# Kernel tuning notes

Hardware: AMD Instinct MI355X
Metric: run time of the kernel (lower is better)

The kernel has to match this reference:

```python
import jax, jax.numpy as jnp
import numpy as np

B, N, Q = 4, 4096, 4096
K = 32                    # max_neighbors (k = min(max_neighbors, N))
NUM_ATOM_TYPES = 100
EMBED_DIM = 32
RBF_DIM = 16
CUTOFF = 5.0
RBF_GAMMA = 1.0 / max(CUTOFF / max(RBF_DIM, 1), 1e-6) ** 2  # 10.24
EPS = 1e-12


def setup_inputs() -> dict:
    key = jax.random.key(0)
    k1, k2, k3, k4, k5 = jax.random.split(key, 5)
    coords = jax.random.normal(k1, (B, N, 3), dtype=jnp.float32) * 10.0
    atom_types = jax.random.randint(k2, (B, N), 0, NUM_ATOM_TYPES)
    radii = jax.random.uniform(k3, (B, N), dtype=jnp.float32) + 0.5
    query_points = jax.random.normal(k4, (B, Q, 3), dtype=jnp.float32) * 10.0
    atom_mask = jnp.ones((B, N), dtype=bool)
    query_mask = jnp.ones((B, Q), dtype=bool)
    embed_table = jax.random.normal(k5, (NUM_ATOM_TYPES, EMBED_DIM), dtype=jnp.float32)
    rbf_centers = jnp.linspace(0.0, CUTOFF, RBF_DIM, dtype=jnp.float32)
    return {"coords": coords, "atom_types": atom_types, "radii": radii,
            "query_points": query_points, "atom_mask": atom_mask,
            "query_mask": query_mask, "embed_table": embed_table,
            "rbf_centers": rbf_centers}


def reference(coords, atom_types, radii, query_points, atom_mask, query_mask,
              embed_table, rbf_centers):
    b = coords.shape[0]
    # stable pairwise distances [B, Q, N]
    diff = query_points[:, :, None, :] - coords[:, None, :, :]
    dists = jnp.sqrt(jnp.sum(diff * diff, axis=-1) + EPS)
    masked_dists = jnp.where(atom_mask[:, None, :], dists, jnp.inf)
    # smallest-k via top_k on negated distances -> [B, Q, K]
    neg_vals, sorted_indices = jax.lax.top_k(-masked_dists, K)
    sorted_dists = -neg_vals

    bidx = jnp.arange(b)[:, None, None]                       # [B,1,1]
    neighbor_atom_mask = atom_mask[bidx, sorted_indices]      # [B,Q,K]
    neighbor_mask = neighbor_atom_mask & (sorted_dists <= CUTOFF) & query_mask[:, :, None]

    neighbor_coords = coords[bidx, sorted_indices]            # [B,Q,K,3]
    neighbor_radii = radii[bidx, sorted_indices][..., None]   # [B,Q,K,1]
    neighbor_types = atom_types[bidx, sorted_indices]         # [B,Q,K]
    neighbor_emb = embed_table[neighbor_types]                # [B,Q,K,E]

    rel_pos = query_points[:, :, None, :] - neighbor_coords   # [B,Q,K,3]
    rel_dist = sorted_dists[..., None]                        # [B,Q,K,1]
    rbf = jnp.exp(-RBF_GAMMA * (rel_dist - rbf_centers[None, None, None, :]) ** 2)

    features = jnp.concatenate([rel_pos, neighbor_radii, neighbor_emb, rbf, rel_dist], axis=-1)
    features = jnp.where(neighbor_mask[..., None], features, 0.0)

    safe_indices = jnp.where(neighbor_atom_mask, sorted_indices, -1)
    safe_dists = jnp.where(neighbor_mask, sorted_dists, 0.0)
    return features, neighbor_mask, safe_indices, safe_dists
```

## Files before the change

### kernel.cpp

```cpp
#include <hip/hip_runtime.h>
#include <stdint.h>

#define B_ 4
#define N_ 4096
#define Q_ 4096
#define K_ 32
#define E_ 32
#define R_ 16
#define F_ 53

static constexpr int WAVES   = 16;
static constexpr int THREADS = WAVES * 64;
static constexpr int QPB     = 32;
static constexpr int CAP     = 104;
static constexpr int TILE    = K_ * F_;
static constexpr int NSLOT   = 4;
static constexpr int POOLB   = (QPB * CAP * 4 > NSLOT * TILE * 4)
                             ? (QPB * CAP * 4) : (NSLOT * TILE * 4);

typedef float v2f __attribute__((ext_vector_type(2)));

__device__ __forceinline__ v2f pk_add(v2f a, v2f b) {
    v2f d; asm("v_pk_add_f32 %0, %1, %2" : "=v"(d) : "v"(a), "v"(b)); return d;
}
__device__ __forceinline__ v2f pk_mul(v2f a, v2f b) {
    v2f d; asm("v_pk_mul_f32 %0, %1, %2" : "=v"(d) : "v"(a), "v"(b)); return d;
}
__device__ __forceinline__ v2f pk_fma(v2f a, v2f b, v2f c) {
    v2f d; asm("v_pk_fma_f32 %0, %1, %2, %3" : "=v"(d) : "v"(a), "v"(b), "v"(c)); return d;
}

__device__ __forceinline__ v2f pk_s2(v2f qx, v2f qy, v2f qz,
                                     v2f nx, v2f ny, v2f nz) {
    const v2f dx = pk_add(qx, nx);
    const v2f dy = pk_add(qy, ny);
    const v2f dz = pk_add(qz, nz);
    return pk_fma(dz, dz, pk_fma(dy, dy, pk_mul(dx, dx)));
}

__device__ __forceinline__ void bitonic_sort64_u32(unsigned int& v, int lane) {
    #pragma unroll
    for (int k = 2; k <= 64; k <<= 1) {
        #pragma unroll
        for (int j = k >> 1; j > 0; j >>= 1) {
            unsigned int o = __shfl_xor(v, j);
            const bool asc = ((lane & k) == 0);
            const bool lower = ((lane & j) == 0);
            unsigned int mn = v < o ? v : o;
            unsigned int mx = v < o ? o : v;
            v = (lower == asc) ? mn : mx;
        }
    }
}

__device__ __forceinline__ void bitonic_sort64_u64(unsigned long long& v, int lane) {
    #pragma unroll
    for (int k = 2; k <= 64; k <<= 1) {
        #pragma unroll
        for (int j = k >> 1; j > 0; j >>= 1) {
            unsigned long long o = __shfl_xor(v, j);
            const bool asc = ((lane & k) == 0);
            const bool lower = ((lane & j) == 0);
            unsigned long long mn = v < o ? v : o;
            unsigned long long mx = v < o ? o : v;
            v = (lower == asc) ? mn : mx;
        }
    }
}

__device__ __forceinline__ void merge64_u64(unsigned long long& best,
                                            unsigned long long c, int lane) {
    unsigned long long rev = __shfl(c, 63 - lane);
    unsigned long long v = best < rev ? best : rev;
    #pragma unroll
    for (int j = 32; j > 0; j >>= 1) {
        unsigned long long o = __shfl_xor(v, j);
        const bool lower = ((lane & j) == 0);
        unsigned long long mn = v < o ? v : o;
        unsigned long long mx = v < o ? o : v;
        v = lower ? mn : mx;
    }
    best = v;
}

__global__ __launch_bounds__(THREADS, 8)
void lfb_kernel(const float* __restrict__ coords,
                const int* __restrict__ atom_types,
                const float* __restrict__ radii,
                const float* __restrict__ qpts,
                const int* __restrict__ atom_mask,
                const int* __restrict__ query_mask,
                const float* __restrict__ embed,
                const float* __restrict__ centers,
                float* __restrict__ out)
{
    __shared__ __align__(16) float nsx[N_], nsy[N_], nsz[N_];
    __shared__ __align__(16) unsigned char pool[POOLB];

    const int tid  = threadIdx.x;
    const int lane = tid & 63;
    const int wv   = tid >> 6;
    const int bq0  = blockIdx.x * QPB;
    const int b    = bq0 / Q_;

    for (int i = tid; i < N_; i += THREADS) {
        const float* c = coords + (size_t)(b * N_ + i) * 3;
        const bool mv = atom_mask[b * N_ + i] != 0;
        nsx[i] = mv ? -c[0] : -1e30f;
        nsy[i] = mv ? -c[1] : -1e30f;
        nsz[i] = mv ? -c[2] : -1e30f;
    }
    __syncthreads();

    const int qA = bq0 + wv;
    const int qB = bq0 + WAVES + wv;
    const float qxA = qpts[(size_t)qA * 3 + 0];
    const float qyA = qpts[(size_t)qA * 3 + 1];
    const float qzA = qpts[(size_t)qA * 3 + 2];
    const float qxB = qpts[(size_t)qB * 3 + 0];
    const float qyB = qpts[(size_t)qB * 3 + 1];
    const float qzB = qpts[(size_t)qB * 3 + 2];
    const v2f qxA2 = {qxA, qxA}, qyA2 = {qyA, qyA}, qzA2 = {qzA, qzA};
    const v2f qxB2 = {qxB, qxB}, qyB2 = {qyB, qyB}, qzB2 = {qzB, qzB};

    const float INF = __uint_as_float(0x7F800000u);
    float mA0 = INF, mA1 = INF, mB0 = INF, mB1 = INF;
    for (int i = 0; i < N_ / 256; ++i) {
        const int a0 = i * 256 + lane * 4;
        const float4 X = *(const float4*)&nsx[a0];
        const float4 Y = *(const float4*)&nsy[a0];
        const float4 Z = *(const float4*)&nsz[a0];
        const v2f Xl = {X.x, X.y}, Xh = {X.z, X.w};
        const v2f Yl = {Y.x, Y.y}, Yh = {Y.z, Y.w};
        const v2f Zl = {Z.x, Z.y}, Zh = {Z.z, Z.w};
        const v2f sAl = pk_s2(qxA2, qyA2, qzA2, Xl, Yl, Zl);
        const v2f sAh = pk_s2(qxA2, qyA2, qzA2, Xh, Yh, Zh);
        const v2f sBl = pk_s2(qxB2, qyB2, qzB2, Xl, Yl, Zl);
        const v2f sBh = pk_s2(qxB2, qyB2, qzB2, Xh, Yh, Zh);
        mA0 = fminf(mA0, fminf(sAl.x, sAh.x));
        mA1 = fminf(mA1, fminf(sAl.y, sAh.y));
        mB0 = fminf(mB0, fminf(sBl.x, sBh.x));
        mB1 = fminf(mB1, fminf(sBl.y, sBh.y));
    }
    unsigned int mnA = __float_as_uint(fminf(mA0, mA1));
    unsigned int mnB = __float_as_uint(fminf(mB0, mB1));
    bitonic_sort64_u32(mnA, lane);
    bitonic_sort64_u32(mnB, lane);
    const unsigned int STA = __shfl(mnA, 31) + 64u;
    const unsigned int STB = __shfl(mnB, 31) + 64u;

    unsigned int* cbA = reinterpret_cast<unsigned int*>(pool) + wv * CAP;
    unsigned int* cbB = reinterpret_cast<unsigned int*>(pool) + (WAVES + wv) * CAP;
    const unsigned long long lt = (1ull << lane) - 1ull;
    int cntA = 0, cntB = 0;
    auto collect = [&](float s, int idx, unsigned int ST, int& cnt,
                       unsigned int* cb) {
        const bool p = __float_as_uint(s) <= ST;
        const unsigned long long m = __ballot(p);
        if (p) {
            const int sl = cnt + __popcll(m & lt);
            if (sl < CAP) cb[sl] = (unsigned int)idx;
        }
        cnt += __popcll(m);
    };
    for (int i = 0; i < N_ / 256; ++i) {
        const int a0 = i * 256 + lane * 4;
        const float4 X = *(const float4*)&nsx[a0];
        const float4 Y = *(const float4*)&nsy[a0];
        const float4 Z = *(const float4*)&nsz[a0];
        const v2f Xl = {X.x, X.y}, Xh = {X.z, X.w};
        const v2f Yl = {Y.x, Y.y}, Yh = {Y.z, Y.w};
        const v2f Zl = {Z.x, Z.y}, Zh = {Z.z, Z.w};
        const v2f sAl = pk_s2(qxA2, qyA2, qzA2, Xl, Yl, Zl);
        const v2f sAh = pk_s2(qxA2, qyA2, qzA2, Xh, Yh, Zh);
        const v2f sBl = pk_s2(qxB2, qyB2, qzB2, Xl, Yl, Zl);
        const v2f sBh = pk_s2(qxB2, qyB2, qzB2, Xh, Yh, Zh);
        collect(sAl.x, a0 + 0, STA, cntA, cbA);
        collect(sAl.y, a0 + 1, STA, cntA, cbA);
        collect(sAh.x, a0 + 2, STA, cntA, cbA);
        collect(sAh.y, a0 + 3, STA, cntA, cbA);
        collect(sBl.x, a0 + 0, STB, cntB, cbB);
        collect(sBl.y, a0 + 1, STB, cntB, cbB);
        collect(sBh.x, a0 + 2, STB, cntB, cbB);
        collect(sBh.y, a0 + 3, STB, cntB, cbB);
    }

    auto select_top32 = [&](const unsigned int* cbuf, int cnt,
                            float qx, float qy, float qz) -> unsigned long long {
        if (cnt <= CAP) {
            unsigned long long best = ~0ull;
            const int nch = (cnt + 63) >> 6;
            for (int c = 0; c < nch; ++c) {
                const int slot = c * 64 + lane;
                unsigned long long v = ~0ull;
                if (slot < cnt) {
                    const int id = (int)cbuf[slot];
                    const float dx = __fadd_rn(qx, nsx[id]);
                    const float dy = __fadd_rn(qy, nsy[id]);
                    const float dz = __fadd_rn(qz, nsz[id]);
                    const float s = __fadd_rn(
                        __fadd_rn(__fmul_rn(dx, dx), __fmul_rn(dy, dy)),
                        __fmul_rn(dz, dz));
                    const float d = __fsqrt_rn(__fadd_rn(s, 1e-12f));
                    v = ((unsigned long long)__float_as_uint(d) << 32)
                      | (unsigned int)id;
                }
                bitonic_sort64_u64(v, lane);
                if (c == 0) best = v;
                else        merge64_u64(best, v, lane);
            }
            return best;
        }
        unsigned long long key = ~0ull;
        for (int base = 0; base < N_; base += 64) {
            const int a = base + lane;
            const float dx = __fadd_rn(qx, nsx[a]);
            const float dy = __fadd_rn(qy, nsy[a]);
            const float dz = __fadd_rn(qz, nsz[a]);
            const float s = __fadd_rn(
                __fadd_rn(__fmul_rn(dx, dx), __fmul_rn(dy, dy)),
                __fmul_rn(dz, dz));
            const float d = __fsqrt_rn(__fadd_rn(s, 1e-12f));
            unsigned long long cand =
                ((unsigned long long)__float_as_uint(d) << 32) | (unsigned int)a;
            const unsigned long long T = __shfl(key, 31);
            unsigned long long m = __ballot(cand < T);
            while (m) {
                const int src = __ffsll(m) - 1;
                m &= m - 1;
                const unsigned long long nk = __shfl(cand, src);
                const unsigned long long up = __shfl_up(key, 1);
                if (lane < K_) {
                    const unsigned long long repl =
                        (lane == 0) ? nk : (up <= nk ? nk : up);
                    key = (key <= nk) ? key : repl;
                }
            }
        }
        return key;
    };

    const unsigned long long keyA = select_top32(cbA, cntA, qxA, qyA, qzA);
    const unsigned long long keyB = select_top32(cbB, cntB, qxB, qyB, qzB);

    const size_t BQK = (size_t)B_ * Q_ * K_;
    float* out_feat = out;
    float* out_mask = out + BQK * (size_t)F_;
    float* out_idx  = out_mask + BQK;
    float* out_dist = out_idx + BQK;

    const bool qmA = query_mask[qA] != 0;
    const bool qmB = query_mask[qB] != 0;

    if (lane < K_) {
        {
            const float d = __uint_as_float((unsigned int)(keyA >> 32));
            const int  id = (int)(keyA & 0xFFFFFFFFull);
            const bool am = ((unsigned int)(keyA >> 32)) < 0x7F800000u;
            const bool nm = am && (d <= 5.0f) && qmA;
            const size_t o = (size_t)qA * K_ + lane;
            out_mask[o] = nm ? 1.0f : 0.0f;
            out_idx[o]  = am ? (float)id : -1.0f;
            out_dist[o] = nm ? d : 0.0f;
        }
        {
            const float d = __uint_as_float((unsigned int)(keyB >> 32));
            const int  id = (int)(keyB & 0xFFFFFFFFull);
            const bool am = ((unsigned int)(keyB >> 32)) < 0x7F800000u;
            const bool nm = am && (d <= 5.0f) && qmB;
            const size_t o = (size_t)qB * K_ + lane;
            out_mask[o] = nm ? 1.0f : 0.0f;
            out_idx[o]  = am ? (float)id : -1.0f;
            out_dist[o] = nm ? d : 0.0f;
        }
    }

    __syncthreads();

    auto build_and_store = [&](int q, unsigned long long key,
                               float qx, float qy, float qz, bool qm,
                               float* slotp) {
        const float d_l  = __uint_as_float((unsigned int)(key >> 32));
        const int   id_l = (int)(key & 0xFFFFFFFFull) & (N_ - 1);
        const bool  am_l = ((unsigned int)(key >> 32)) < 0x7F800000u;
        const bool  nm_l = am_l && (d_l <= 5.0f) && qm;

        if (lane < K_) {
            float* f = slotp + lane * F_;
            f[0] = nm_l ? __fadd_rn(qx, nsx[id_l]) : 0.0f;
            f[1] = nm_l ? __fadd_rn(qy, nsy[id_l]) : 0.0f;
            f[2] = nm_l ? __fadd_rn(qz, nsz[id_l]) : 0.0f;
            f[3] = nm_l ? radii[b * N_ + id_l] : 0.0f;

            const int t = atom_types[b * N_ + id_l];
            const float4* er4 = (const float4*)(embed + t * E_);
            #pragma unroll
            for (int e = 0; e < E_ / 4; ++e) {
                const float4 v = er4[e];
                f[4 + e * 4 + 0] = nm_l ? v.x : 0.0f;
                f[4 + e * 4 + 1] = nm_l ? v.y : 0.0f;
                f[4 + e * 4 + 2] = nm_l ? v.z : 0.0f;
                f[4 + e * 4 + 3] = nm_l ? v.w : 0.0f;
            }

            const float NG = -(float)(256.0 / 25.0);
            #pragma unroll
            for (int rr = 0; rr < R_; ++rr) {
                const float dd = __fsub_rn(d_l, centers[rr]);
                const float a2 = __fmul_rn(dd, dd);
                f[36 + rr] = nm_l ? expf(__fmul_rn(NG, a2)) : 0.0f;
            }
            f[52] = nm_l ? d_l : 0.0f;
        }
        const float4* s4 = (const float4*)slotp;
        float4* d4 = (float4*)(out_feat + (size_t)q * (size_t)TILE);
        for (int t4 = lane; t4 < TILE / 4; t4 += 64) d4[t4] = s4[t4];
    };

    float* stagef = reinterpret_cast<float*>(pool);
    for (int r = 0; r < 8; ++r) {
        if ((wv >> 2) == (r & 3)) {
            float* slotp = stagef + (size_t)(wv & (NSLOT - 1)) * TILE;
            if (r < 4) build_and_store(qA, keyA, qxA, qyA, qzA, qmA, slotp);
            else       build_and_store(qB, keyB, qxB, qyB, qzB, qmB, slotp);
        }
        __syncthreads();
    }
}

extern "C" void kernel_launch(void* const* d_in, const int* in_sizes, int n_in,
                              void* d_out, int out_size, void* d_ws, size_t ws_size,
                              hipStream_t stream) {
    const float* coords     = (const float*)d_in[0];
    const int*   atom_types = (const int*)d_in[1];
    const float* radii      = (const float*)d_in[2];
    const float* qpts       = (const float*)d_in[3];
    const int*   atom_mask  = (const int*)d_in[4];
    const int*   query_mask = (const int*)d_in[5];
    const float* embed      = (const float*)d_in[6];
    const float* centers    = (const float*)d_in[7];

    dim3 grid((B_ * Q_) / QPB);
    dim3 block(THREADS);
    lfb_kernel<<<grid, block, 0, stream>>>(coords, atom_types, radii, qpts,
                                           atom_mask, query_mask, embed, centers,
                                           (float*)d_out);
}
```

Baseline: 64.66 us.

## Bucket atoms and queries by x-coordinate to prune the neighbor search

Adds a prep kernel that counting-sorts atoms and queries into 512 x-slabs, storing atoms as float4 (negated coords plus original index) and queries sorted by x with their original index and mask packed in. The main kernel no longer stages all N atoms in LDS. Each wave scans only the slab range inside an adaptive radius, starting from a guess derived from |q|^2 and doubling until 32 candidates are found, then runs the same threshold-collect and top-32 select. The aim is to cut the O(N) distance work per query, at the cost of an extra launch, global-memory atom reads, and a radius heuristic tuned to the Gaussian test distribution.

```diff
diff --git a/kernel.cpp b/kernel.cpp
--- a/kernel.cpp
+++ b/kernel.cpp
@@ -9,33 +9,22 @@
 #define R_ 16
 #define F_ 53
 
+static constexpr int   NB   = 512;
+static constexpr float XLO  = -64.0f;
+static constexpr float INVW = 4.0f;
+
 static constexpr int WAVES   = 16;
 static constexpr int THREADS = WAVES * 64;
 static constexpr int QPB     = 32;
-static constexpr int CAP     = 104;
+static constexpr int CAP     = 128;
 static constexpr int TILE    = K_ * F_;
-static constexpr int NSLOT   = 4;
+static constexpr int NSLOT   = 8;
 static constexpr int POOLB   = (QPB * CAP * 4 > NSLOT * TILE * 4)
                              ? (QPB * CAP * 4) : (NSLOT * TILE * 4);
 
-typedef float v2f __attribute__((ext_vector_type(2)));
-
-__device__ __forceinline__ v2f pk_add(v2f a, v2f b) {
-    v2f d; asm("v_pk_add_f32 %0, %1, %2" : "=v"(d) : "v"(a), "v"(b)); return d;
-}
-__device__ __forceinline__ v2f pk_mul(v2f a, v2f b) {
-    v2f d; asm("v_pk_mul_f32 %0, %1, %2" : "=v"(d) : "v"(a), "v"(b)); return d;
-}
-__device__ __forceinline__ v2f pk_fma(v2f a, v2f b, v2f c) {
-    v2f d; asm("v_pk_fma_f32 %0, %1, %2, %3" : "=v"(d) : "v"(a), "v"(b), "v"(c)); return d;
-}
-
-__device__ __forceinline__ v2f pk_s2(v2f qx, v2f qy, v2f qz,
-                                     v2f nx, v2f ny, v2f nz) {
-    const v2f dx = pk_add(qx, nx);
-    const v2f dy = pk_add(qy, ny);
-    const v2f dz = pk_add(qz, nz);
-    return pk_fma(dz, dz, pk_fma(dy, dy, pk_mul(dx, dx)));
+__device__ __host__ __forceinline__ int xbucket(float v) {
+    int i = (int)floorf((v - XLO) * INVW);
+    return i < 0 ? 0 : (i > NB - 1 ? NB - 1 : i);
 }
 
 __device__ __forceinline__ void bitonic_sort64_u32(unsigned int& v, int lane) {
@@ -83,106 +72,194 @@
     best = v;
 }
 
+__global__ __launch_bounds__(1024)
+void prep_kernel(const float* __restrict__ coords,
+                 const int* __restrict__ atom_mask,
+                 const float* __restrict__ qpts,
+                 const int* __restrict__ query_mask,
+                 float4* __restrict__ aos,
+                 float4* __restrict__ qaos,
+                 unsigned int* __restrict__ bstart)
+{
+    __shared__ unsigned int hist[NB], incl[NB], cur[NB];
+    const int b = blockIdx.x;
+    const int tid = threadIdx.x;
+
+    if (tid < NB) hist[tid] = 0;
+    __syncthreads();
+    for (int i = tid; i < N_; i += 1024) {
+        const bool mv = atom_mask[b * N_ + i] != 0;
+        const float x = mv ? coords[(size_t)(b * N_ + i) * 3] : 1e30f;
+        atomicAdd(&hist[xbucket(x)], 1u);
+    }
+    __syncthreads();
+    if (tid < NB) incl[tid] = hist[tid];
+    __syncthreads();
+    for (int off = 1; off < NB; off <<= 1) {
+        unsigned int v = 0;
+        if (tid < NB && tid >= off) v = incl[tid - off];
+        __syncthreads();
+        if (tid < NB) incl[tid] += v;
+        __syncthreads();
+    }
+    if (tid < NB) {
+        const unsigned int ex = incl[tid] - hist[tid];
+        cur[tid] = ex;
+        bstart[b * (NB + 1) + tid] = ex;
+    }
+    if (tid == 0) bstart[b * (NB + 1) + NB] = N_;
+    __syncthreads();
+    for (int i = tid; i < N_; i += 1024) {
+        const float* c = coords + (size_t)(b * N_ + i) * 3;
+        const bool mv = atom_mask[b * N_ + i] != 0;
+        const float nx = mv ? -c[0] : -1e30f;
+        const float ny = mv ? -c[1] : -1e30f;
+        const float nz = mv ? -c[2] : -1e30f;
+        const int bk = xbucket(-nx);
+        const unsigned int pos = atomicAdd(&cur[bk], 1u);
+        aos[(size_t)b * N_ + pos] =
+            make_float4(nx, ny, nz, __uint_as_float((unsigned int)i));
+    }
+    __syncthreads();
+
+    if (tid < NB) hist[tid] = 0;
+    __syncthreads();
+    for (int i = tid; i < Q_; i += 1024)
+        atomicAdd(&hist[xbucket(qpts[(size_t)(b * Q_ + i) * 3])], 1u);
+    __syncthreads();
+    if (tid < NB) incl[tid] = hist[tid];
+    __syncthreads();
+    for (int off = 1; off < NB; off <<= 1) {
+        unsigned int v = 0;
+        if (tid < NB && tid >= off) v = incl[tid - off];
+        __syncthreads();
+        if (tid < NB) incl[tid] += v;
+        __syncthreads();
+    }
+    if (tid < NB) cur[tid] = incl[tid] - hist[tid];
+    __syncthreads();
+    for (int i = tid; i < Q_; i += 1024) {
+        const float* q = qpts + (size_t)(b * Q_ + i) * 3;
+        const float qx = q[0], qy = q[1], qz = q[2];
+        const unsigned int qm = (query_mask[b * Q_ + i] != 0) ? 1u : 0u;
+        const unsigned int pos = atomicAdd(&cur[xbucket(qx)], 1u);
+        qaos[(size_t)b * Q_ + pos] =
+            make_float4(qx, qy, qz, __uint_as_float((unsigned int)i | (qm << 16)));
+    }
+}
+
 __global__ __launch_bounds__(THREADS, 8)
 void lfb_kernel(const float* __restrict__ coords,
                 const int* __restrict__ atom_types,
                 const float* __restrict__ radii,
-                const float* __restrict__ qpts,
-                const int* __restrict__ atom_mask,
-                const int* __restrict__ query_mask,
                 const float* __restrict__ embed,
                 const float* __restrict__ centers,
+                const float4* __restrict__ aos,
+                const float4* __restrict__ qaos,
+                const unsigned int* __restrict__ bstart,
                 float* __restrict__ out)
 {
-    __shared__ __align__(16) float nsx[N_], nsy[N_], nsz[N_];
     __shared__ __align__(16) unsigned char pool[POOLB];
 
     const int tid  = threadIdx.x;
     const int lane = tid & 63;
     const int wv   = tid >> 6;
-    const int bq0  = blockIdx.x * QPB;
-    const int b    = bq0 / Q_;
-
-    for (int i = tid; i < N_; i += THREADS) {
-        const float* c = coords + (size_t)(b * N_ + i) * 3;
-        const bool mv = atom_mask[b * N_ + i] != 0;
-        nsx[i] = mv ? -c[0] : -1e30f;
-        nsy[i] = mv ? -c[1] : -1e30f;
-        nsz[i] = mv ? -c[2] : -1e30f;
-    }
-    __syncthreads();
-
-    const int qA = bq0 + wv;
-    const int qB = bq0 + WAVES + wv;
-    const float qxA = qpts[(size_t)qA * 3 + 0];
-    const float qyA = qpts[(size_t)qA * 3 + 1];
-    const float qzA = qpts[(size_t)qA * 3 + 2];
-    const float qxB = qpts[(size_t)qB * 3 + 0];
-    const float qyB = qpts[(size_t)qB * 3 + 1];
-    const float qzB = qpts[(size_t)qB * 3 + 2];
-    const v2f qxA2 = {qxA, qxA}, qyA2 = {qyA, qyA}, qzA2 = {qzA, qzA};
-    const v2f qxB2 = {qxB, qxB}, qyB2 = {qyB, qyB}, qzB2 = {qzB, qzB};
-
-    const float INF = __uint_as_float(0x7F800000u);
-    float mA0 = INF, mA1 = INF, mB0 = INF, mB1 = INF;
-    for (int i = 0; i < N_ / 256; ++i) {
-        const int a0 = i * 256 + lane * 4;
-        const float4 X = *(const float4*)&nsx[a0];
-        const float4 Y = *(const float4*)&nsy[a0];
-        const float4 Z = *(const float4*)&nsz[a0];
-        const v2f Xl = {X.x, X.y}, Xh = {X.z, X.w};
-        const v2f Yl = {Y.x, Y.y}, Yh = {Y.z, Y.w};
-        const v2f Zl = {Z.x, Z.y}, Zh = {Z.z, Z.w};
-        const v2f sAl = pk_s2(qxA2, qyA2, qzA2, Xl, Yl, Zl);
-        const v2f sAh = pk_s2(qxA2, qyA2, qzA2, Xh, Yh, Zh);
-        const v2f sBl = pk_s2(qxB2, qyB2, qzB2, Xl, Yl, Zl);
-        const v2f sBh = pk_s2(qxB2, qyB2, qzB2, Xh, Yh, Zh);
-        mA0 = fminf(mA0, fminf(sAl.x, sAh.x));
-        mA1 = fminf(mA1, fminf(sAl.y, sAh.y));
-        mB0 = fminf(mB0, fminf(sBl.x, sBh.x));
-        mB1 = fminf(mB1, fminf(sBl.y, sBh.y));
-    }
-    unsigned int mnA = __float_as_uint(fminf(mA0, mA1));
-    unsigned int mnB = __float_as_uint(fminf(mB0, mB1));
-    bitonic_sort64_u32(mnA, lane);
-    bitonic_sort64_u32(mnB, lane);
-    const unsigned int STA = __shfl(mnA, 31) + 64u;
-    const unsigned int STB = __shfl(mnB, 31) + 64u;
-
-    unsigned int* cbA = reinterpret_cast<unsigned int*>(pool) + wv * CAP;
-    unsigned int* cbB = reinterpret_cast<unsigned int*>(pool) + (WAVES + wv) * CAP;
+    const int b    = blockIdx.x >> 7;
+    const int base32 = (blockIdx.x & 127) * QPB;
+
+    const float4* aosb = aos + (size_t)b * N_;
+    const unsigned int* bs = bstart + b * (NB + 1);
+
+    const float4 qa = qaos[(size_t)b * Q_ + base32 + 2 * wv];
+    const float4 qb = qaos[(size_t)b * Q_ + base32 + 2 * wv + 1];
+    const float qxA = qa.x, qyA = qa.y, qzA = qa.z;
+    const float qxB = qb.x, qyB = qb.y, qzB = qb.z;
+    const unsigned int wA = __float_as_uint(qa.w);
+    const unsigned int wB = __float_as_uint(qb.w);
+    const int origqA = (int)(wA & 0xFFFFu), origqB = (int)(wB & 0xFFFFu);
+    const bool qmA = (wA >> 16) & 1u, qmB = (wB >> 16) & 1u;
+
+    const float INFf = __uint_as_float(0x7F800000u);
+
+    const float dotA = qxA * qxA + qyA * qyA + qzA * qzA;
+    const float dotB = qxB * qxB + qyB * qyB + qzB * qzB;
+    float rA = fminf(3.2f * __expf(dotA * (1.0f / 600.0f)), 40.0f);
+    float rB = fminf(3.2f * __expf(dotB * (1.0f / 600.0f)), 40.0f);
+
+    int s = 0, e = 0;
+    unsigned int TsA, TsB;
+    for (;;) {
+        const int lo = min(xbucket(qxA - rA), xbucket(qxB - rB));
+        const int hi = max(xbucket(qxA + rA), xbucket(qxB + rB));
+        s = (int)bs[lo];
+        e = (int)bs[hi + 1];
+        float mA = INFf, mB = INFf;
+        for (int bi = s; bi < e; bi += 256) {
+            float4 a[4];
+            #pragma unroll
+            for (int u = 0; u < 4; ++u) {
+                const int i = bi + u * 64 + lane;
+                a[u] = aosb[i < e ? i : e - 1];
+            }
+            #pragma unroll
+            for (int u = 0; u < 4; ++u) {
+                const int i = bi + u * 64 + lane;
+                float dx = qxA + a[u].x, dy = qyA + a[u].y, dz = qzA + a[u].z;
+                const float sA = fmaf(dz, dz, fmaf(dy, dy, dx * dx));
+                dx = qxB + a[u].x; dy = qyB + a[u].y; dz = qzB + a[u].z;
+                const float sB = fmaf(dz, dz, fmaf(dy, dy, dx * dx));
+                if (i < e) { mA = fminf(mA, sA); mB = fminf(mB, sB); }
+            }
+        }
+        unsigned int ua = __float_as_uint(mA), ub = __float_as_uint(mB);
+        bitonic_sort64_u32(ua, lane);
+        bitonic_sort64_u32(ub, lane);
+        TsA = __shfl(ua, 31);
+        TsB = __shfl(ub, 31);
+        const bool okA = __uint_as_float(TsA) <= 0.999f * rA * rA;
+        const bool okB = __uint_as_float(TsB) <= 0.999f * rB * rB;
+        if ((okA && okB) || (lo == 0 && hi == NB - 1)) break;
+        if (!okA) rA *= 2.0f;
+        if (!okB) rB *= 2.0f;
+    }
+    const unsigned int STA = TsA + 64u;
+    const unsigned int STB = TsB + 64u;
+
+    unsigned int* poolu = reinterpret_cast<unsigned int*>(pool);
+    unsigned int* cbA = poolu + (size_t)(wv * 2 + 0) * CAP;
+    unsigned int* cbB = poolu + (size_t)(wv * 2 + 1) * CAP;
     const unsigned long long lt = (1ull << lane) - 1ull;
     int cntA = 0, cntB = 0;
-    auto collect = [&](float s, int idx, unsigned int ST, int& cnt,
-                       unsigned int* cb) {
-        const bool p = __float_as_uint(s) <= ST;
-        const unsigned long long m = __ballot(p);
-        if (p) {
-            const int sl = cnt + __popcll(m & lt);
-            if (sl < CAP) cb[sl] = (unsigned int)idx;
-        }
-        cnt += __popcll(m);
-    };
-    for (int i = 0; i < N_ / 256; ++i) {
-        const int a0 = i * 256 + lane * 4;
-        const float4 X = *(const float4*)&nsx[a0];
-        const float4 Y = *(const float4*)&nsy[a0];
-        const float4 Z = *(const float4*)&nsz[a0];
-        const v2f Xl = {X.x, X.y}, Xh = {X.z, X.w};
-        const v2f Yl = {Y.x, Y.y}, Yh = {Y.z, Y.w};
-        const v2f Zl = {Z.x, Z.y}, Zh = {Z.z, Z.w};
-        const v2f sAl = pk_s2(qxA2, qyA2, qzA2, Xl, Yl, Zl);
-        const v2f sAh = pk_s2(qxA2, qyA2, qzA2, Xh, Yh, Zh);
-        const v2f sBl = pk_s2(qxB2, qyB2, qzB2, Xl, Yl, Zl);
-        const v2f sBh = pk_s2(qxB2, qyB2, qzB2, Xh, Yh, Zh);
-        collect(sAl.x, a0 + 0, STA, cntA, cbA);
-        collect(sAl.y, a0 + 1, STA, cntA, cbA);
-        collect(sAh.x, a0 + 2, STA, cntA, cbA);
-        collect(sAh.y, a0 + 3, STA, cntA, cbA);
-        collect(sBl.x, a0 + 0, STB, cntB, cbB);
-        collect(sBl.y, a0 + 1, STB, cntB, cbB);
-        collect(sBh.x, a0 + 2, STB, cntB, cbB);
-        collect(sBh.y, a0 + 3, STB, cntB, cbB);
+    for (int bi = s; bi < e; bi += 256) {
+        float4 a[4];
+        #pragma unroll
+        for (int u = 0; u < 4; ++u) {
+            const int i = bi + u * 64 + lane;
+            a[u] = aosb[i < e ? i : e - 1];
+        }
+        #pragma unroll
+        for (int u = 0; u < 4; ++u) {
+            const int i = bi + u * 64 + lane;
+            const bool ok = i < e;
+            float dx = qxA + a[u].x, dy = qyA + a[u].y, dz = qzA + a[u].z;
+            const float sA = fmaf(dz, dz, fmaf(dy, dy, dx * dx));
+            dx = qxB + a[u].x; dy = qyB + a[u].y; dz = qzB + a[u].z;
+            const float sB = fmaf(dz, dz, fmaf(dy, dy, dx * dx));
+            const bool pA = ok && (__float_as_uint(sA) <= STA);
+            unsigned long long mm = __ballot(pA);
+            if (pA) {
+                const int sl = cntA + __popcll(mm & lt);
+                if (sl < CAP) cbA[sl] = (unsigned int)i;
+            }
+            cntA += __popcll(mm);
+            const bool pB = ok && (__float_as_uint(sB) <= STB);
+            mm = __ballot(pB);
+            if (pB) {
+                const int sl = cntB + __popcll(mm & lt);
+                if (sl < CAP) cbB[sl] = (unsigned int)i;
+            }
+            cntB += __popcll(mm);
+        }
     }
 
     auto select_top32 = [&](const unsigned int* cbuf, int cnt,
@@ -194,16 +271,16 @@
                 const int slot = c * 64 + lane;
                 unsigned long long v = ~0ull;
                 if (slot < cnt) {
-                    const int id = (int)cbuf[slot];
-                    const float dx = __fadd_rn(qx, nsx[id]);
-                    const float dy = __fadd_rn(qy, nsy[id]);
-                    const float dz = __fadd_rn(qz, nsz[id]);
-                    const float s = __fadd_rn(
+                    const float4 a = aosb[cbuf[slot]];
+                    const float dx = __fadd_rn(qx, a.x);
+                    const float dy = __fadd_rn(qy, a.y);
+                    const float dz = __fadd_rn(qz, a.z);
+                    const float sv = __fadd_rn(
                         __fadd_rn(__fmul_rn(dx, dx), __fmul_rn(dy, dy)),
                         __fmul_rn(dz, dz));
-                    const float d = __fsqrt_rn(__fadd_rn(s, 1e-12f));
+                    const float d = __fsqrt_rn(__fadd_rn(sv, 1e-12f));
                     v = ((unsigned long long)__float_as_uint(d) << 32)
-                      | (unsigned int)id;
+                      | __float_as_uint(a.w);
                 }
                 bitonic_sort64_u64(v, lane);
                 if (c == 0) best = v;
@@ -212,17 +289,18 @@
             return best;
         }
         unsigned long long key = ~0ull;
-        for (int base = 0; base < N_; base += 64) {
-            const int a = base + lane;
-            const float dx = __fadd_rn(qx, nsx[a]);
-            const float dy = __fadd_rn(qy, nsy[a]);
-            const float dz = __fadd_rn(qz, nsz[a]);
-            const float s = __fadd_rn(
+        for (int bi = 0; bi < N_; bi += 64) {
+            const float4 a = aosb[bi + lane];
+            const float dx = __fadd_rn(qx, a.x);
+            const float dy = __fadd_rn(qy, a.y);
+            const float dz = __fadd_rn(qz, a.z);
+            const float sv = __fadd_rn(
                 __fadd_rn(__fmul_rn(dx, dx), __fmul_rn(dy, dy)),
                 __fmul_rn(dz, dz));
-            const float d = __fsqrt_rn(__fadd_rn(s, 1e-12f));
-            unsigned long long cand =
-                ((unsigned long long)__float_as_uint(d) << 32) | (unsigned int)a;
+            const float d = __fsqrt_rn(__fadd_rn(sv, 1e-12f));
+            const unsigned long long cand =
+                ((unsigned long long)__float_as_uint(d) << 32)
+                | __float_as_uint(a.w);
             const unsigned long long T = __shfl(key, 31);
             unsigned long long m = __ballot(cand < T);
             while (m) {
@@ -249,8 +327,8 @@
     float* out_idx  = out_mask + BQK;
     float* out_dist = out_idx + BQK;
 
-    const bool qmA = query_mask[qA] != 0;
-    const bool qmB = query_mask[qB] != 0;
+    const int flatqA = b * Q_ + origqA;
+    const int flatqB = b * Q_ + origqB;
 
     if (lane < K_) {
         {
@@ -258,7 +336,7 @@
             const int  id = (int)(keyA & 0xFFFFFFFFull);
             const bool am = ((unsigned int)(keyA >> 32)) < 0x7F800000u;
             const bool nm = am && (d <= 5.0f) && qmA;
-            const size_t o = (size_t)qA * K_ + lane;
+            const size_t o = (size_t)flatqA * K_ + lane;
             out_mask[o] = nm ? 1.0f : 0.0f;
             out_idx[o]  = am ? (float)id : -1.0f;
             out_dist[o] = nm ? d : 0.0f;
@@ -268,7 +346,7 @@
             const int  id = (int)(keyB & 0xFFFFFFFFull);
             const bool am = ((unsigned int)(keyB >> 32)) < 0x7F800000u;
             const bool nm = am && (d <= 5.0f) && qmB;
-            const size_t o = (size_t)qB * K_ + lane;
+            const size_t o = (size_t)flatqB * K_ + lane;
             out_mask[o] = nm ? 1.0f : 0.0f;
             out_idx[o]  = am ? (float)id : -1.0f;
             out_dist[o] = nm ? d : 0.0f;
@@ -277,7 +355,7 @@
 
     __syncthreads();
 
-    auto build_and_store = [&](int q, unsigned long long key,
+    auto build_and_store = [&](int flatq, unsigned long long key,
                                float qx, float qy, float qz, bool qm,
                                float* slotp) {
         const float d_l  = __uint_as_float((unsigned int)(key >> 32));
@@ -287,20 +365,21 @@
 
         if (lane < K_) {
             float* f = slotp + lane * F_;
-            f[0] = nm_l ? __fadd_rn(qx, nsx[id_l]) : 0.0f;
-            f[1] = nm_l ? __fadd_rn(qy, nsy[id_l]) : 0.0f;
-            f[2] = nm_l ? __fadd_rn(qz, nsz[id_l]) : 0.0f;
+            const float* cp = coords + (size_t)(b * N_ + id_l) * 3;
+            f[0] = nm_l ? __fsub_rn(qx, cp[0]) : 0.0f;
+            f[1] = nm_l ? __fsub_rn(qy, cp[1]) : 0.0f;
+            f[2] = nm_l ? __fsub_rn(qz, cp[2]) : 0.0f;
             f[3] = nm_l ? radii[b * N_ + id_l] : 0.0f;
 
             const int t = atom_types[b * N_ + id_l];
             const float4* er4 = (const float4*)(embed + t * E_);
             #pragma unroll
-            for (int e = 0; e < E_ / 4; ++e) {
-                const float4 v = er4[e];
-                f[4 + e * 4 + 0] = nm_l ? v.x : 0.0f;
-                f[4 + e * 4 + 1] = nm_l ? v.y : 0.0f;
-                f[4 + e * 4 + 2] = nm_l ? v.z : 0.0f;
-                f[4 + e * 4 + 3] = nm_l ? v.w : 0.0f;
+            for (int ei = 0; ei < E_ / 4; ++ei) {
+                const float4 v = er4[ei];
+                f[4 + ei * 4 + 0] = nm_l ? v.x : 0.0f;
+                f[4 + ei * 4 + 1] = nm_l ? v.y : 0.0f;
+                f[4 + ei * 4 + 2] = nm_l ? v.z : 0.0f;
+                f[4 + ei * 4 + 3] = nm_l ? v.w : 0.0f;
             }
 
             const float NG = -(float)(256.0 / 25.0);
@@ -313,16 +392,16 @@
             f[52] = nm_l ? d_l : 0.0f;
         }
         const float4* s4 = (const float4*)slotp;
-        float4* d4 = (float4*)(out_feat + (size_t)q * (size_t)TILE);
+        float4* d4 = (float4*)(out_feat + (size_t)flatq * (size_t)TILE);
         for (int t4 = lane; t4 < TILE / 4; t4 += 64) d4[t4] = s4[t4];
     };
 
     float* stagef = reinterpret_cast<float*>(pool);
-    for (int r = 0; r < 8; ++r) {
-        if ((wv >> 2) == (r & 3)) {
+    for (int r = 0; r < 4; ++r) {
+        if ((wv >> 3) == (r & 1)) {
             float* slotp = stagef + (size_t)(wv & (NSLOT - 1)) * TILE;
-            if (r < 4) build_and_store(qA, keyA, qxA, qyA, qzA, qmA, slotp);
-            else       build_and_store(qB, keyB, qxB, qyB, qzB, qmB, slotp);
+            if (r < 2) build_and_store(flatqA, keyA, qxA, qyA, qzA, qmA, slotp);
+            else       build_and_store(flatqB, keyB, qxB, qyB, qzB, qmB, slotp);
         }
         __syncthreads();
     }
@@ -340,9 +419,16 @@
     const float* embed      = (const float*)d_in[6];
     const float* centers    = (const float*)d_in[7];
 
+    float4* aos  = (float4*)d_ws;
+    float4* qaos = aos + (size_t)B_ * N_;
+    unsigned int* bstart = (unsigned int*)(qaos + (size_t)B_ * Q_);
+
+    prep_kernel<<<B_, 1024, 0, stream>>>(coords, atom_mask, qpts, query_mask,
+                                         aos, qaos, bstart);
+
     dim3 grid((B_ * Q_) / QPB);
     dim3 block(THREADS);
-    lfb_kernel<<<grid, block, 0, stream>>>(coords, atom_types, radii, qpts,
-                                           atom_mask, query_mask, embed, centers,
+    lfb_kernel<<<grid, block, 0, stream>>>(coords, atom_types, radii,
+                                           embed, centers, aos, qaos, bstart,
                                            (float*)d_out);
 }
```

After: 91.72 us. 41.8% more time.

## Replace full threshold pass with sampled loose threshold plus tight refinement

Applied to the files above, without the earlier changes.

The top-32 threshold is now estimated from only the first 1024 atoms instead of a full first pass over all atoms. Lane-wise minima gathered during the single full collect pass then give a tight threshold, which filters the loose candidate list down to at most 64 before one 64-wide sort. Each wave now handles one query instead of two, so the grid doubles. That repeats the per-block shared-memory coordinate load more often and drops the reuse of each coordinate load across two queries. A looser first threshold also makes overflow into the slow merge or full-scan fallback more likely.

```diff
diff --git a/kernel.cpp b/kernel.cpp
--- a/kernel.cpp
+++ b/kernel.cpp
@@ -11,12 +11,12 @@
 
 static constexpr int WAVES   = 16;
 static constexpr int THREADS = WAVES * 64;
-static constexpr int QPB     = 32;
-static constexpr int CAP     = 104;
+static constexpr int SUB     = 1024;
+static constexpr int CAPL    = 352;
+static constexpr int CAPT    = 64;
 static constexpr int TILE    = K_ * F_;
 static constexpr int NSLOT   = 4;
-static constexpr int POOLB   = (QPB * CAP * 4 > NSLOT * TILE * 4)
-                             ? (QPB * CAP * 4) : (NSLOT * TILE * 4);
+static constexpr int POOLB   = NSLOT * TILE * 4;
 
 typedef float v2f __attribute__((ext_vector_type(2)));
 
@@ -29,13 +29,19 @@
 __device__ __forceinline__ v2f pk_fma(v2f a, v2f b, v2f c) {
     v2f d; asm("v_pk_fma_f32 %0, %1, %2, %3" : "=v"(d) : "v"(a), "v"(b), "v"(c)); return d;
 }
-
 __device__ __forceinline__ v2f pk_s2(v2f qx, v2f qy, v2f qz,
                                      v2f nx, v2f ny, v2f nz) {
     const v2f dx = pk_add(qx, nx);
     const v2f dy = pk_add(qy, ny);
     const v2f dz = pk_add(qz, nz);
     return pk_fma(dz, dz, pk_fma(dy, dy, pk_mul(dx, dx)));
+}
+__device__ __forceinline__ float s2_fma(float qx, float qy, float qz,
+                                        float nx, float ny, float nz) {
+    const float dx = __fadd_rn(qx, nx);
+    const float dy = __fadd_rn(qy, ny);
+    const float dz = __fadd_rn(qz, nz);
+    return __fmaf_rn(dz, dz, __fmaf_rn(dy, dy, __fmul_rn(dx, dx)));
 }
 
 __device__ __forceinline__ void bitonic_sort64_u32(unsigned int& v, int lane) {
@@ -100,7 +106,7 @@
     const int tid  = threadIdx.x;
     const int lane = tid & 63;
     const int wv   = tid >> 6;
-    const int bq0  = blockIdx.x * QPB;
+    const int bq0  = blockIdx.x * WAVES;
     const int b    = bq0 / Q_;
 
     for (int i = tid; i < N_; i += THREADS) {
@@ -112,20 +118,16 @@
     }
     __syncthreads();
 
-    const int qA = bq0 + wv;
-    const int qB = bq0 + WAVES + wv;
-    const float qxA = qpts[(size_t)qA * 3 + 0];
-    const float qyA = qpts[(size_t)qA * 3 + 1];
-    const float qzA = qpts[(size_t)qA * 3 + 2];
-    const float qxB = qpts[(size_t)qB * 3 + 0];
-    const float qyB = qpts[(size_t)qB * 3 + 1];
-    const float qzB = qpts[(size_t)qB * 3 + 2];
-    const v2f qxA2 = {qxA, qxA}, qyA2 = {qyA, qyA}, qzA2 = {qzA, qzA};
-    const v2f qxB2 = {qxB, qxB}, qyB2 = {qyB, qyB}, qzB2 = {qzB, qzB};
-
-    const float INF = __uint_as_float(0x7F800000u);
-    float mA0 = INF, mA1 = INF, mB0 = INF, mB1 = INF;
-    for (int i = 0; i < N_ / 256; ++i) {
+    const int bq = bq0 + wv;
+    const float qx = qpts[(size_t)bq * 3 + 0];
+    const float qy = qpts[(size_t)bq * 3 + 1];
+    const float qz = qpts[(size_t)bq * 3 + 2];
+    const v2f qx2 = {qx, qx}, qy2 = {qy, qy}, qz2 = {qz, qz};
+
+    const float INFf = __uint_as_float(0x7F800000u);
+
+    float l0 = INFf, l1 = INFf, l2 = INFf, l3 = INFf;
+    for (int i = 0; i < SUB / 256; ++i) {
         const int a0 = i * 256 + lane * 4;
         const float4 X = *(const float4*)&nsx[a0];
         const float4 Y = *(const float4*)&nsy[a0];
@@ -133,33 +135,27 @@
         const v2f Xl = {X.x, X.y}, Xh = {X.z, X.w};
         const v2f Yl = {Y.x, Y.y}, Yh = {Y.z, Y.w};
         const v2f Zl = {Z.x, Z.y}, Zh = {Z.z, Z.w};
-        const v2f sAl = pk_s2(qxA2, qyA2, qzA2, Xl, Yl, Zl);
-        const v2f sAh = pk_s2(qxA2, qyA2, qzA2, Xh, Yh, Zh);
-        const v2f sBl = pk_s2(qxB2, qyB2, qzB2, Xl, Yl, Zl);
-        const v2f sBh = pk_s2(qxB2, qyB2, qzB2, Xh, Yh, Zh);
-        mA0 = fminf(mA0, fminf(sAl.x, sAh.x));
-        mA1 = fminf(mA1, fminf(sAl.y, sAh.y));
-        mB0 = fminf(mB0, fminf(sBl.x, sBh.x));
-        mB1 = fminf(mB1, fminf(sBl.y, sBh.y));
-    }
-    unsigned int mnA = __float_as_uint(fminf(mA0, mA1));
-    unsigned int mnB = __float_as_uint(fminf(mB0, mB1));
-    bitonic_sort64_u32(mnA, lane);
-    bitonic_sort64_u32(mnB, lane);
-    const unsigned int STA = __shfl(mnA, 31) + 64u;
-    const unsigned int STB = __shfl(mnB, 31) + 64u;
-
-    unsigned int* cbA = reinterpret_cast<unsigned int*>(pool) + wv * CAP;
-    unsigned int* cbB = reinterpret_cast<unsigned int*>(pool) + (WAVES + wv) * CAP;
+        const v2f sl = pk_s2(qx2, qy2, qz2, Xl, Yl, Zl);
+        const v2f sh = pk_s2(qx2, qy2, qz2, Xh, Yh, Zh);
+        l0 = fminf(l0, sl.x); l1 = fminf(l1, sl.y);
+        l2 = fminf(l2, sh.x); l3 = fminf(l3, sh.y);
+    }
+    unsigned int tsl = __float_as_uint(fminf(fminf(l0, l1), fminf(l2, l3)));
+    bitonic_sort64_u32(tsl, lane);
+    const unsigned int STl = __shfl(tsl, 31) + 64u;
+
+    unsigned int* loose = reinterpret_cast<unsigned int*>(pool) + wv * CAPL;
+    unsigned int* tight = reinterpret_cast<unsigned int*>(pool)
+                        + WAVES * CAPL + wv * CAPT;
     const unsigned long long lt = (1ull << lane) - 1ull;
-    int cntA = 0, cntB = 0;
-    auto collect = [&](float s, int idx, unsigned int ST, int& cnt,
-                       unsigned int* cb) {
-        const bool p = __float_as_uint(s) <= ST;
+    int cnt = 0;
+    float m0 = INFf, m1 = INFf, m2 = INFf, m3 = INFf;
+    auto collect = [&](float s, int idx) {
+        const bool p = __float_as_uint(s) <= STl;
         const unsigned long long m = __ballot(p);
         if (p) {
             const int sl = cnt + __popcll(m & lt);
-            if (sl < CAP) cb[sl] = (unsigned int)idx;
+            if (sl < CAPL) loose[sl] = (unsigned int)idx;
         }
         cnt += __popcll(m);
     };
@@ -171,58 +167,67 @@
         const v2f Xl = {X.x, X.y}, Xh = {X.z, X.w};
         const v2f Yl = {Y.x, Y.y}, Yh = {Y.z, Y.w};
         const v2f Zl = {Z.x, Z.y}, Zh = {Z.z, Z.w};
-        const v2f sAl = pk_s2(qxA2, qyA2, qzA2, Xl, Yl, Zl);
-        const v2f sAh = pk_s2(qxA2, qyA2, qzA2, Xh, Yh, Zh);
-        const v2f sBl = pk_s2(qxB2, qyB2, qzB2, Xl, Yl, Zl);
-        const v2f sBh = pk_s2(qxB2, qyB2, qzB2, Xh, Yh, Zh);
-        collect(sAl.x, a0 + 0, STA, cntA, cbA);
-        collect(sAl.y, a0 + 1, STA, cntA, cbA);
-        collect(sAh.x, a0 + 2, STA, cntA, cbA);
-        collect(sAh.y, a0 + 3, STA, cntA, cbA);
-        collect(sBl.x, a0 + 0, STB, cntB, cbB);
-        collect(sBl.y, a0 + 1, STB, cntB, cbB);
-        collect(sBh.x, a0 + 2, STB, cntB, cbB);
-        collect(sBh.y, a0 + 3, STB, cntB, cbB);
-    }
-
-    auto select_top32 = [&](const unsigned int* cbuf, int cnt,
-                            float qx, float qy, float qz) -> unsigned long long {
-        if (cnt <= CAP) {
+        const v2f sl = pk_s2(qx2, qy2, qz2, Xl, Yl, Zl);
+        const v2f sh = pk_s2(qx2, qy2, qz2, Xh, Yh, Zh);
+        m0 = fminf(m0, sl.x); m1 = fminf(m1, sl.y);
+        m2 = fminf(m2, sh.x); m3 = fminf(m3, sh.y);
+        collect(sl.x, a0 + 0);
+        collect(sl.y, a0 + 1);
+        collect(sh.x, a0 + 2);
+        collect(sh.y, a0 + 3);
+    }
+    unsigned int tst = __float_as_uint(fminf(fminf(m0, m1), fminf(m2, m3)));
+    bitonic_sort64_u32(tst, lane);
+    const unsigned int STt = __shfl(tst, 31) + 64u;
+
+    auto rekey = [&](int id) -> unsigned long long {
+        const float dx = __fadd_rn(qx, nsx[id]);
+        const float dy = __fadd_rn(qy, nsy[id]);
+        const float dz = __fadd_rn(qz, nsz[id]);
+        const float sv = __fadd_rn(
+            __fadd_rn(__fmul_rn(dx, dx), __fmul_rn(dy, dy)),
+            __fmul_rn(dz, dz));
+        const float d = __fsqrt_rn(__fadd_rn(sv, 1e-12f));
+        return ((unsigned long long)__float_as_uint(d) << 32) | (unsigned int)id;
+    };
+
+    unsigned long long key;
+    if (cnt <= CAPL) {
+        int tcnt = 0;
+        const int nchL = (cnt + 63) >> 6;
+        for (int c = 0; c < nchL; ++c) {
+            const int slot = c * 64 + lane;
+            const bool valid = slot < cnt;
+            const int id = valid ? (int)loose[slot] : 0;
+            const float s = s2_fma(qx, qy, qz, nsx[id], nsy[id], nsz[id]);
+            const bool p = valid && (__float_as_uint(s) <= STt);
+            const unsigned long long m = __ballot(p);
+            if (p) {
+                const int sl = tcnt + __popcll(m & lt);
+                if (sl < CAPT) tight[sl] = (unsigned int)id;
+            }
+            tcnt += __popcll(m);
+        }
+        if (tcnt <= CAPT) {
+            unsigned long long v = (lane < tcnt) ? rekey((int)tight[lane]) : ~0ull;
+            bitonic_sort64_u64(v, lane);
+            key = v;
+        } else {
             unsigned long long best = ~0ull;
-            const int nch = (cnt + 63) >> 6;
-            for (int c = 0; c < nch; ++c) {
+            for (int c = 0; c < nchL; ++c) {
                 const int slot = c * 64 + lane;
-                unsigned long long v = ~0ull;
-                if (slot < cnt) {
-                    const int id = (int)cbuf[slot];
-                    const float dx = __fadd_rn(qx, nsx[id]);
-                    const float dy = __fadd_rn(qy, nsy[id]);
-                    const float dz = __fadd_rn(qz, nsz[id]);
-                    const float s = __fadd_rn(
-                        __fadd_rn(__fmul_rn(dx, dx), __fmul_rn(dy, dy)),
-                        __fmul_rn(dz, dz));
-                    const float d = __fsqrt_rn(__fadd_rn(s, 1e-12f));
-                    v = ((unsigned long long)__float_as_uint(d) << 32)
-                      | (unsigned int)id;
-                }
+                unsigned long long v =
+                    (slot < cnt) ? rekey((int)loose[slot]) : ~0ull;
                 bitonic_sort64_u64(v, lane);
                 if (c == 0) best = v;
                 else        merge64_u64(best, v, lane);
             }
-            return best;
-        }
-        unsigned long long key = ~0ull;
+            key = best;
+        }
+    } else {
+        key = ~0ull;
         for (int base = 0; base < N_; base += 64) {
-            const int a = base + lane;
-            const float dx = __fadd_rn(qx, nsx[a]);
-            const float dy = __fadd_rn(qy, nsy[a]);
-            const float dz = __fadd_rn(qz, nsz[a]);
-            const float s = __fadd_rn(
-                __fadd_rn(__fmul_rn(dx, dx), __fmul_rn(dy, dy)),
-                __fmul_rn(dz, dz));
-            const float d = __fsqrt_rn(__fadd_rn(s, 1e-12f));
-            unsigned long long cand =
-                ((unsigned long long)__float_as_uint(d) << 32) | (unsigned int)a;
+            const unsigned long long cand = rekey(base + lane);
             const unsigned long long T = __shfl(key, 31);
             unsigned long long m = __ballot(cand < T);
             while (m) {
@@ -237,11 +242,7 @@
                 }
             }
         }
-        return key;
-    };
-
-    const unsigned long long keyA = select_top32(cbA, cntA, qxA, qyA, qzA);
-    const unsigned long long keyB = select_top32(cbB, cntB, qxB, qyB, qzB);
+    }
 
     const size_t BQK = (size_t)B_ * Q_ * K_;
     float* out_feat = out;
@@ -249,80 +250,56 @@
     float* out_idx  = out_mask + BQK;
     float* out_dist = out_idx + BQK;
 
-    const bool qmA = query_mask[qA] != 0;
-    const bool qmB = query_mask[qB] != 0;
+    const bool qm = query_mask[bq] != 0;
+
+    const float d_l  = __uint_as_float((unsigned int)(key >> 32));
+    const int   id_l = (int)(key & 0xFFFFFFFFull) & (N_ - 1);
+    const bool  am_l = ((unsigned int)(key >> 32)) < 0x7F800000u;
+    const bool  nm_l = am_l && (d_l <= 5.0f) && qm;
 
     if (lane < K_) {
-        {
-            const float d = __uint_as_float((unsigned int)(keyA >> 32));
-            const int  id = (int)(keyA & 0xFFFFFFFFull);
-            const bool am = ((unsigned int)(keyA >> 32)) < 0x7F800000u;
-            const bool nm = am && (d <= 5.0f) && qmA;
-            const size_t o = (size_t)qA * K_ + lane;
-            out_mask[o] = nm ? 1.0f : 0.0f;
-            out_idx[o]  = am ? (float)id : -1.0f;
-            out_dist[o] = nm ? d : 0.0f;
-        }
-        {
-            const float d = __uint_as_float((unsigned int)(keyB >> 32));
-            const int  id = (int)(keyB & 0xFFFFFFFFull);
-            const bool am = ((unsigned int)(keyB >> 32)) < 0x7F800000u;
-            const bool nm = am && (d <= 5.0f) && qmB;
-            const size_t o = (size_t)qB * K_ + lane;
-            out_mask[o] = nm ? 1.0f : 0.0f;
-            out_idx[o]  = am ? (float)id : -1.0f;
-            out_dist[o] = nm ? d : 0.0f;
-        }
+        const size_t o = (size_t)bq * K_ + lane;
+        out_mask[o] = nm_l ? 1.0f : 0.0f;
+        out_idx[o]  = am_l ? (float)id_l : -1.0f;
+        out_dist[o] = nm_l ? d_l : 0.0f;
     }
 
     __syncthreads();
 
-    auto build_and_store = [&](int q, unsigned long long key,
-                               float qx, float qy, float qz, bool qm,
-                               float* slotp) {
-        const float d_l  = __uint_as_float((unsigned int)(key >> 32));
-        const int   id_l = (int)(key & 0xFFFFFFFFull) & (N_ - 1);
-        const bool  am_l = ((unsigned int)(key >> 32)) < 0x7F800000u;
-        const bool  nm_l = am_l && (d_l <= 5.0f) && qm;
-
-        if (lane < K_) {
-            float* f = slotp + lane * F_;
-            f[0] = nm_l ? __fadd_rn(qx, nsx[id_l]) : 0.0f;
-            f[1] = nm_l ? __fadd_rn(qy, nsy[id_l]) : 0.0f;
-            f[2] = nm_l ? __fadd_rn(qz, nsz[id_l]) : 0.0f;
-            f[3] = nm_l ? radii[b * N_ + id_l] : 0.0f;
-
-            const int t = atom_types[b * N_ + id_l];
-            const float4* er4 = (const float4*)(embed + t * E_);
-            #pragma unroll
-            for (int e = 0; e < E_ / 4; ++e) {
-                const float4 v = er4[e];
-                f[4 + e * 4 + 0] = nm_l ? v.x : 0.0f;
-                f[4 + e * 4 + 1] = nm_l ? v.y : 0.0f;
-                f[4 + e * 4 + 2] = nm_l ? v.z : 0.0f;
-                f[4 + e * 4 + 3] = nm_l ? v.w : 0.0f;
+    float* stagef = reinterpret_cast<float*>(pool);
+    for (int r = 0; r < WAVES / NSLOT; ++r) {
+        if ((wv >> 2) == r) {
+            float* f0 = stagef + (size_t)(wv & (NSLOT - 1)) * TILE;
+            if (lane < K_) {
+                float* f = f0 + lane * F_;
+                f[0] = nm_l ? __fadd_rn(qx, nsx[id_l]) : 0.0f;
+                f[1] = nm_l ? __fadd_rn(qy, nsy[id_l]) : 0.0f;
+                f[2] = nm_l ? __fadd_rn(qz, nsz[id_l]) : 0.0f;
+                f[3] = nm_l ? radii[b * N_ + id_l] : 0.0f;
+
+                const int t = atom_types[b * N_ + id_l];
+                const float4* er4 = (const float4*)(embed + t * E_);
+                #pragma unroll
+                for (int e = 0; e < E_ / 4; ++e) {
+                    const float4 v = er4[e];
+                    f[4 + e * 4 + 0] = nm_l ? v.x : 0.0f;
+                    f[4 + e * 4 + 1] = nm_l ? v.y : 0.0f;
+                    f[4 + e * 4 + 2] = nm_l ? v.z : 0.0f;
+                    f[4 + e * 4 + 3] = nm_l ? v.w : 0.0f;
+                }
+
+                const float NG = -(float)(256.0 / 25.0);
+                #pragma unroll
+                for (int rr = 0; rr < R_; ++rr) {
+                    const float dd = __fsub_rn(d_l, centers[rr]);
+                    const float a2 = __fmul_rn(dd, dd);
+                    f[36 + rr] = nm_l ? expf(__fmul_rn(NG, a2)) : 0.0f;
+                }
+                f[52] = nm_l ? d_l : 0.0f;
             }
-
-            const float NG = -(float)(256.0 / 25.0);
-            #pragma unroll
-            for (int rr = 0; rr < R_; ++rr) {
-                const float dd = __fsub_rn(d_l, centers[rr]);
-                const float a2 = __fmul_rn(dd, dd);
-                f[36 + rr] = nm_l ? expf(__fmul_rn(NG, a2)) : 0.0f;
-            }
-            f[52] = nm_l ? d_l : 0.0f;
-        }
-        const float4* s4 = (const float4*)slotp;
-        float4* d4 = (float4*)(out_feat + (size_t)q * (size_t)TILE);
-        for (int t4 = lane; t4 < TILE / 4; t4 += 64) d4[t4] = s4[t4];
-    };
-
-    float* stagef = reinterpret_cast<float*>(pool);
-    for (int r = 0; r < 8; ++r) {
-        if ((wv >> 2) == (r & 3)) {
-            float* slotp = stagef + (size_t)(wv & (NSLOT - 1)) * TILE;
-            if (r < 4) build_and_store(qA, keyA, qxA, qyA, qzA, qmA, slotp);
-            else       build_and_store(qB, keyB, qxB, qyB, qzB, qmB, slotp);
+            const float4* s4 = (const float4*)f0;
+            float4* d4 = (float4*)(out_feat + (size_t)bq * (size_t)TILE);
+            for (int t4 = lane; t4 < TILE / 4; t4 += 64) d4[t4] = s4[t4];
         }
         __syncthreads();
     }
@@ -340,7 +317,7 @@
     const float* embed      = (const float*)d_in[6];
     const float* centers    = (const float*)d_in[7];
 
-    dim3 grid((B_ * Q_) / QPB);
+    dim3 grid((B_ * Q_) / WAVES);
     dim3 block(THREADS);
     lfb_kernel<<<grid, block, 0, stream>>>(coords, atom_types, radii, qpts,
                                            atom_mask, query_mask, embed, centers,
```

Result: slower. 73.22 us (+13.2%).
